# Kernel tuning notes

Hardware: AMD Instinct MI355X
Metric: run time of the kernel (lower is better)

## Reference

```python
import jax, jax.numpy as jnp
import numpy as np
from jax import lax

INPUT_SIZE = 512
THRESHOLD = 0.5
IOU_TH = 0.3
MAX_ROIS = 32   # py_cpu_nms(...)[:32]
ROI = 7
NEG = jnp.float32(-1e30)


def _make_anchors(fh, fw, stride):
    # 3 scales x 3 ratios = 9 anchors per cell, laid out in (h, w, anchor)
    # order to match permute(0,2,3,1).view(-1) of the conv heads.
    scales = np.array([32.0, 64.0, 128.0])
    ratios = np.array([0.5, 1.0, 2.0])
    ws = (scales[:, None] * np.sqrt(ratios)[None, :]).reshape(-1)
    hs = (scales[:, None] / np.sqrt(ratios)[None, :]).reshape(-1)
    cy = (np.arange(fh) + 0.5) * stride
    cx = (np.arange(fw) + 0.5) * stride
    CX, CY = np.meshgrid(cx, cy)
    CX = CX[..., None]; CY = CY[..., None]
    a = np.stack([CX - ws / 2, CY - hs / 2, CX + ws / 2, CY + hs / 2], axis=-1)
    return jnp.asarray(a.reshape(-1, 4), jnp.float32)


def setup_inputs() -> dict:
    key = jax.random.key(0)
    k1, k2, k3 = jax.random.split(key, 3)
    B, C, FH, FW, A, stride = 4, 256, 64, 64, 9, 8
    featureMap = jax.random.normal(k1, (B, C, FH, FW), jnp.float32)
    # small init so sigmoid scores spread across threshold and exp(tw) stays sane
    w_cls = jax.random.normal(k2, (A, C, 3, 3), jnp.float32) * 0.05
    w_loc = jax.random.normal(k3, (4 * A, C, 3, 3), jnp.float32) * 0.01
    prior_anchor = _make_anchors(FH, FW, stride)
    return {"featureMap": featureMap, "prior_anchor": prior_anchor,
            "w_cls": w_cls, "w_loc": w_loc, "stride": stride}


def _conv(x, w):
    return lax.conv_general_dilated(x, w, (1, 1), "SAME",
                                    dimension_numbers=("NCHW", "OIHW", "NCHW"))


def _decode(loc, anchors):
    aw = anchors[:, 2] - anchors[:, 0]
    ah = anchors[:, 3] - anchors[:, 1]
    acx = anchors[:, 0] + 0.5 * aw
    acy = anchors[:, 1] + 0.5 * ah
    cx = acx + loc[:, 0] * aw
    cy = acy + loc[:, 1] * ah
    w = aw * jnp.exp(loc[:, 2])
    h = ah * jnp.exp(loc[:, 3])
    return jnp.stack([cx - 0.5 * w, cy - 0.5 * h, cx + 0.5 * w, cy + 0.5 * h], axis=1)


def _iou_one(box, boxes):
    xx1 = jnp.maximum(box[0], boxes[:, 0]); yy1 = jnp.maximum(box[1], boxes[:, 1])
    xx2 = jnp.minimum(box[2], boxes[:, 2]); yy2 = jnp.minimum(box[3], boxes[:, 3])
    inter = jnp.clip(xx2 - xx1, 0) * jnp.clip(yy2 - yy1, 0)
    a1 = (box[2] - box[0]) * (box[3] - box[1])
    a2 = (boxes[:, 2] - boxes[:, 0]) * (boxes[:, 3] - boxes[:, 1])
    return inter / (a1 + a2 - inter + 1e-9)


def _nms(boxes, scores, valid):
    # greedy NMS, fixed MAX_ROIS rounds (== sort-by-score py_cpu_nms + [:32])
    N = scores.shape[0]
    s0 = jnp.where(valid, scores, -1.0)

    def body(i, carry):
        s, picks, ok = carry
        idx = jnp.argmax(s)
        good = s[idx] > 0.0
        picks = picks.at[i].set(idx.astype(jnp.int32))
        ok = ok.at[i].set(good)
        sup = (_iou_one(boxes[idx], boxes) > IOU_TH) | (jnp.arange(N) == idx)
        return (jnp.where(sup, -1.0, s), picks, ok)

    _, picks, ok = lax.fori_loop(
        0, MAX_ROIS, body,
        (s0, jnp.zeros(MAX_ROIS, jnp.int32), jnp.zeros(MAX_ROIS, bool)))
    return picks, ok


def _ceil_div(a, b):
    return -(-a // b)


def _adaptive_maxpool(feat, box):
    # feat: [C, FH, FW]; box: int32 [x1, y1, x2, y2] in feature-map coords.
    # Faithful F.adaptive_max_pool2d bins: start=floor(i*h/7), end=ceil((i+1)*h/7).
    FH, FW = feat.shape[1], feat.shape[2]
    x1, y1, x2, y2 = box[0], box[1], box[2], box[3]
    h = y2 - y1; w = x2 - x1
    i = jnp.arange(ROI)
    rs = y1 + (i * h) // ROI; re = y1 + _ceil_div((i + 1) * h, ROI)
    cs = x1 + (i * w) // ROI; ce = x1 + _ceil_div((i + 1) * w, ROI)
    hh = jnp.arange(FH); ww = jnp.arange(FW)
    rm = jnp.where((hh >= rs[:, None]) & (hh < re[:, None]), 0.0, NEG)  # [7, FH]
    cm = jnp.where((ww >= cs[:, None]) & (ww < ce[:, None]), 0.0, NEG)  # [7, FW]
    t = jnp.max(feat[None] + rm[:, None, :, None], axis=2)              # [7, C, FW]
    out = jnp.max(t[:, None] + cm[None, :, None, :], axis=3)            # [7, 7, C]
    return jnp.transpose(out, (2, 0, 1))                                # [C, 7, 7]


def reference(featureMap, prior_anchor, w_cls, w_loc, stride):
    B, C, FH, FW = featureMap.shape
    cls = jax.nn.sigmoid(_conv(featureMap, w_cls))                      # [B, A, FH, FW]
    cls = jnp.transpose(cls, (0, 2, 3, 1)).reshape(B, -1)               # [B, N]
    loc = jnp.transpose(_conv(featureMap, w_loc), (0, 2, 3, 1)).reshape(B, -1, 4)
    boxes = jax.vmap(_decode, in_axes=(0, None))(loc, prior_anchor)     # [B, N, 4]
    boxes = jnp.clip(boxes, 0.0, float(INPUT_SIZE))                     # clamp(0, input_size)
    valid = (cls > THRESHOLD) \
          & (boxes[..., 2] - boxes[..., 0] >= 2 * stride) \
          & (boxes[..., 3] - boxes[..., 1] >= 2 * stride)
    picks, ok = jax.vmap(_nms)(boxes, cls, valid)                       # [B, 32]
    sel_boxes = jnp.take_along_axis(boxes, picks[..., None], axis=1)    # [B, 32, 4]
    sel_scores = jnp.take_along_axis(cls, picks, axis=1)                # [B, 32]
    eval_boxes = jnp.where(
        ok[..., None],
        jnp.concatenate([sel_boxes, sel_scores[..., None]], axis=-1), 0.0)
    # src_coordinate.int() / stride -> integer feature-map coords
    ib = sel_boxes.astype(jnp.int32) // stride
    fx1 = jnp.clip(ib[..., 0], 0, FW - 1); fy1 = jnp.clip(ib[..., 1], 0, FH - 1)
    fx2 = jnp.clip(ib[..., 2], fx1 + 1, FW); fy2 = jnp.clip(ib[..., 3], fy1 + 1, FH)
    fb = jnp.stack([fx1, fy1, fx2, fy2], axis=-1).reshape(-1, 4)        # [B*32, 4]
    img = jnp.repeat(jnp.arange(B), MAX_ROIS)
    rois = lax.map(lambda a: _adaptive_maxpool(featureMap[a[1]], a[0]), (fb, img))
    rois = jnp.where(ok.reshape(-1)[:, None, None, None], rois, 0.0)    # [B*32, 256, 7, 7]
    return eval_boxes, ok, rois
```

## Files before the change

### kernel.cpp

```cpp
#include <hip/hip_runtime.h>
#include <hip/hip_bf16.h>

#define FHH 64
#define FWW 64
#define CIN 256
#define NB 4
#define NA 9
#define NANCH 36864
#define NPOS 4096
#define OC_TOTAL 45
#define OCP 48
#define MAXROIS 32
#define ROI 7
#define NEGV -1e30f
#define NCHUNK 576
#define NTH 16
#define CAP 1024

typedef unsigned long long u64;

__device__ __constant__ const float TH_LADDER[NTH] = {
    0.9999f, 0.9998f, 0.9995f, 0.999f, 0.998f, 0.997f, 0.995f, 0.993f,
    0.99f, 0.987f, 0.984f, 0.98f, 0.975f, 0.97f, 0.96f, 0.0f};

__device__ __forceinline__ void pick_threshold(
    const int* __restrict__ gcnt, int b, int cap,
    float* T, int* C, int* V, int* frc)
{
    int bestc = 0; float bt = TH_LADDER[0];
#pragma unroll
    for (int i = 0; i < NTH; ++i) {
        int c = gcnt[b * NTH + i];
        if (c <= cap && c > bestc) { bestc = c; bt = TH_LADDER[i]; }
    }
    int f = (gcnt[b * NTH + 0] > cap) ? 1 : 0;
    if (f) { bestc = cap; bt = TH_LADDER[0]; }
    *T = bt; *C = bestc; *V = gcnt[b * NTH + NTH - 1]; *frc = f;
}

__global__ __launch_bounds__(256) void wtrans_kernel(
    const float* __restrict__ wcls,
    const float* __restrict__ wloc,
    float* __restrict__ wT,
    int* __restrict__ gcnt)
{
    if (blockIdx.x == 0 && threadIdx.x < NB * NTH) gcnt[threadIdx.x] = 0;
    int idx = blockIdx.x * 256 + threadIdx.x;
    int o = idx % 48;
    int rest = idx / 48;
    int tap = rest % 9;
    int c = rest / 9;
    float v = 0.f;
    if (o < OC_TOTAL) {
        v = (o < NA) ? wcls[((size_t)o * CIN + c) * 9 + tap]
                     : wloc[((size_t)(o - NA) * CIN + c) * 9 + tap];
    }
    wT[idx] = v;
}

__global__ __launch_bounds__(256) void conv_kernel(
    const float* __restrict__ feat,
    const float* __restrict__ wT,
    float* __restrict__ partial,
    int nkg, int cpk)
{
    __shared__ float flds[16][18][20];

    int blk = blockIdx.x;
    int low = blk & 7;
    int rest = blk >> 3;
    int kg = rest % nkg;
    int uhi = rest / nkg;
    int unit = uhi * 8 + low;
    int b = unit >> 4;
    int tile = unit & 15;

    int ty0 = (tile >> 2) * 16;
    int tx0 = (tile & 3) * 16;

    int pb = threadIdx.x & 63;
    int q = __builtin_amdgcn_readfirstlane(threadIdx.x >> 6);
    int ry0 = (pb >> 3) * 2;
    int rx0 = (pb & 7) * 2;

    int cbase = kg * cpk;

    float acc[2][2][12];
#pragma unroll
    for (int py = 0; py < 2; ++py)
#pragma unroll
        for (int px = 0; px < 2; ++px)
#pragma unroll
            for (int o = 0; o < 12; ++o) acc[py][px][o] = 0.f;

    for (int c0 = 0; c0 < cpk; c0 += 16) {
        __syncthreads();
        for (int idx = threadIdx.x; idx < 16 * 324; idx += 256) {
            int c = idx / 324;
            int r = idx - c * 324;
            int y = r / 18;
            int x = r - y * 18;
            int gy = ty0 + y - 1;
            int gx = tx0 + x - 1;
            float v = 0.f;
            if ((unsigned)gy < FHH && (unsigned)gx < FWW)
                v = feat[((size_t)(b * CIN + cbase + c0 + c) * FHH + gy) * FWW + gx];
            flds[c][y][x] = v;
        }
        __syncthreads();

        const float* wq = wT + (size_t)(cbase + c0) * 432 + q * 12;
        for (int c = 0; c < 16; ++c) {
            float f[4][4];
#pragma unroll
            for (int r = 0; r < 4; ++r) {
                float2 a0 = *(const float2*)&flds[c][ry0 + r][rx0];
                float2 a1 = *(const float2*)&flds[c][ry0 + r][rx0 + 2];
                f[r][0] = a0.x; f[r][1] = a0.y; f[r][2] = a1.x; f[r][3] = a1.y;
            }
#pragma unroll
            for (int tap = 0; tap < 9; ++tap) {
                int dy = tap / 3, dx = tap % 3;
                const float* wp = wq + (c * 9 + tap) * 48;
                float w[12];
#pragma unroll
                for (int o = 0; o < 12; ++o) w[o] = wp[o];
#pragma unroll
                for (int py = 0; py < 2; ++py)
#pragma unroll
                for (int px = 0; px < 2; ++px) {
                    float fv = f[py + dy][px + dx];
#pragma unroll
                    for (int o = 0; o < 12; ++o)
                        acc[py][px][o] += fv * w[o];
                }
            }
        }
    }

    float* pout = partial + ((size_t)kg * NB + b) * OCP * NPOS;
#pragma unroll
    for (int o = 0; o < 12; ++o) {
        int oo = q * 12 + o;
        if (oo >= OC_TOTAL) continue;
        float* op = pout + (size_t)oo * NPOS;
#pragma unroll
        for (int py = 0; py < 2; ++py)
#pragma unroll
        for (int px = 0; px < 2; ++px) {
            int pos = (ty0 + ry0 + py) * FWW + (tx0 + rx0 + px);
            op[pos] = acc[py][px][o];
        }
    }
}

__global__ __launch_bounds__(256) void decode_kernel(
    const float* __restrict__ partial,
    const float* __restrict__ anchors,
    const int* __restrict__ stridep,
    float* __restrict__ boxes,
    float* __restrict__ scores,
    int* __restrict__ gcnt,
    int* __restrict__ gcount,
    int nkg)
{
    __shared__ int hcnt[NTH];
    if (threadIdx.x < NTH) hcnt[threadIdx.x] = 0;
    if (blockIdx.x == 0 && threadIdx.x < NB) gcount[threadIdx.x] = 0;
    __syncthreads();

    int t = blockIdx.x * 256 + threadIdx.x;
    int pos = t & (NPOS - 1);
    int ba = t >> 12;
    int b = ba / 9;
    int a = ba - b * 9;

    float cls = 0.f, l0 = 0.f, l1 = 0.f, l2 = 0.f, l3 = 0.f;
    for (int kg = 0; kg < nkg; ++kg) {
        const float* pk = partial + ((size_t)kg * NB + b) * OCP * NPOS;
        cls += pk[(size_t)a * NPOS + pos];
        l0 += pk[(size_t)(NA + a * 4 + 0) * NPOS + pos];
        l1 += pk[(size_t)(NA + a * 4 + 1) * NPOS + pos];
        l2 += pk[(size_t)(NA + a * 4 + 2) * NPOS + pos];
        l3 += pk[(size_t)(NA + a * 4 + 3) * NPOS + pos];
    }

    float sig = 1.f / (1.f + expf(-cls));
    int n = pos * NA + a;
    const float* an = anchors + (size_t)n * 4;
    float ax1 = an[0], ay1 = an[1], ax2 = an[2], ay2 = an[3];
    float aw = ax2 - ax1, ah = ay2 - ay1;
    float acx = ax1 + 0.5f * aw, acy = ay1 + 0.5f * ah;
    float cx = acx + l0 * aw;
    float cy = acy + l1 * ah;
    float w = aw * expf(l2);
    float h = ah * expf(l3);
    float x1 = fminf(fmaxf(cx - 0.5f * w, 0.f), 512.f);
    float y1 = fminf(fmaxf(cy - 0.5f * h, 0.f), 512.f);
    float x2 = fminf(fmaxf(cx + 0.5f * w, 0.f), 512.f);
    float y2 = fminf(fmaxf(cy + 0.5f * h, 0.f), 512.f);
    int stride = stridep[0];
    float msz = 2.f * (float)stride;
    bool valid = (sig > 0.5f) && ((x2 - x1) >= msz) && ((y2 - y1) >= msz);
    ((float4*)boxes)[(size_t)b * NANCH + n] = make_float4(x1, y1, x2, y2);
    scores[(size_t)b * NANCH + n] = valid ? sig : -1.0f;

#pragma unroll
    for (int i = 0; i < NTH; ++i) {
        u64 mb = __ballot(valid && sig >= TH_LADDER[i]);
        if ((threadIdx.x & 63) == 0 && mb)
            atomicAdd(&hcnt[i], (int)__popcll(mb));
    }
    __syncthreads();
    if (threadIdx.x < NTH && hcnt[threadIdx.x])
        atomicAdd(&gcnt[b * NTH + threadIdx.x], hcnt[threadIdx.x]);
}

__global__ __launch_bounds__(256) void nms_compact_kernel(
    const float* __restrict__ scores,
    const int* __restrict__ gcnt,
    int* __restrict__ gcount,
    u64* __restrict__ candkey,
    int cap)
{
    __shared__ int lcnt;
    __shared__ int wbase[4];
    __shared__ int gbase;
    int t = blockIdx.x * 256 + threadIdx.x;
    int b = t / NANCH;
    int j = t - b * NANCH;
    int lane = threadIdx.x & 63;
    int w = threadIdx.x >> 6;
    if (threadIdx.x == 0) lcnt = 0;
    __syncthreads();

    float T; int C, V, frc;
    pick_threshold(gcnt, b, cap, &T, &C, &V, &frc);

    float v = scores[t];
    bool p = (v > 0.f) && (v >= T);
    u64 m = __ballot(p);
    int cnt = (int)__popcll(m);
    if (lane == 0) wbase[w] = atomicAdd(&lcnt, cnt);
    __syncthreads();
    if (threadIdx.x == 0) gbase = lcnt ? atomicAdd(&gcount[b], lcnt) : 0;
    __syncthreads();
    if (p) {
        int off = (int)__popcll(m & ((1ULL << lane) - 1ULL));
        int slot = gbase + wbase[w] + off;
        if (slot < cap)
            candkey[(size_t)b * cap + slot] =
                ((u64)__float_as_uint(v) << 32) | (unsigned int)(~j);
    }
}

__device__ __forceinline__ void write_outputs(
    int b, int i, bool okv, int idx, float sc,
    const float4* Bb4, const int* stridep,
    float* d_out, int* ifb, int* iok)
{
    float4 bb = Bb4[idx];
    float* eb = d_out + ((size_t)b * MAXROIS + i) * 5;
    eb[0] = okv ? bb.x : 0.f;
    eb[1] = okv ? bb.y : 0.f;
    eb[2] = okv ? bb.z : 0.f;
    eb[3] = okv ? bb.w : 0.f;
    eb[4] = okv ? sc : 0.f;
    d_out[NB * MAXROIS * 5 + b * MAXROIS + i] = okv ? 1.f : 0.f;
    int st = stridep[0];
    int fx1 = min(max(((int)bb.x) / st, 0), FWW - 1);
    int fy1 = min(max(((int)bb.y) / st, 0), FHH - 1);
    int fx2 = min(max(((int)bb.z) / st, fx1 + 1), FWW);
    int fy2 = min(max(((int)bb.w) / st, fy1 + 1), FHH);
    int r = b * MAXROIS + i;
    ifb[r * 4 + 0] = fx1;
    ifb[r * 4 + 1] = fy1;
    ifb[r * 4 + 2] = fx2;
    ifb[r * 4 + 3] = fy2;
    iok[r] = okv ? 1 : 0;
}

__global__ __launch_bounds__(512) void nms_sortscan_kernel(
    const u64* __restrict__ candkey,
    const float* __restrict__ boxes,
    const int* __restrict__ gcnt,
    const int* __restrict__ stridep,
    float* __restrict__ d_out,
    int* __restrict__ ifb, int* __restrict__ iok, int* __restrict__ flag,
    int cap)
{
    __shared__ u64 skey[CAP];
    __shared__ float4 box_l[CAP];
    __shared__ u64 mask[CAP / 64];
    __shared__ int picks[MAXROIS];
    __shared__ int np_sh;

    int b = blockIdx.x;
    int tid = threadIdx.x;
    int lane = tid & 63;
    if (tid == 0) np_sh = 0;

    float T; int C, V, frc;
    pick_threshold(gcnt, b, cap, &T, &C, &V, &frc);

    int CSZ = 64;
    while (CSZ < C) CSZ <<= 1;

    for (int j = tid; j < CSZ; j += 512)
        skey[j] = (j < C) ? candkey[(size_t)b * cap + j] : 0ULL;

    int prev_cross = 1;
    for (int kk = 2; kk <= CSZ; kk <<= 1) {
        for (int jj = kk >> 1; jj > 0; jj >>= 1) {
            int cross = (jj >= 128) ? 1 : 0;
            if (cross || prev_cross) __syncthreads();
            for (int tt = tid; tt < (CSZ >> 1); tt += 512) {
                int i = ((tt & ~(jj - 1)) << 1) | (tt & (jj - 1));
                int l = i + jj;
                u64 a = skey[i], c2 = skey[l];
                bool up = ((i & kk) == 0);
                bool sw = up ? (a < c2) : (a > c2);
                if (sw) { skey[i] = c2; skey[l] = a; }
            }
            prev_cross = cross;
        }
    }
    __syncthreads();

    const float4* Bb4 = (const float4*)(boxes + (size_t)b * NANCH * 4);
    for (int j = tid; j < C; j += 512) {
        int id = (int)(~((unsigned int)(skey[j] & 0xFFFFFFFFULL)));
        box_l[j] = Bb4[id];
    }
    if (tid < CAP / 64) {
        int base = tid * 64;
        u64 m0;
        if (base >= C) m0 = ~0ULL;
        else if (base + 64 > C) m0 = ~((1ULL << (C - base)) - 1ULL);
        else m0 = 0ULL;
        mask[tid] = m0;
    }
    __syncthreads();

    for (int round = 0; round < MAXROIS; ++round) {
        u64 mw = (lane < CAP / 64) ? mask[lane] : ~0ULL;
        int bpos = __ffsll((u64)(~mw));
        int cand = bpos ? lane * 64 + bpos - 1 : 0x7FFFFFFF;
#pragma unroll
        for (int off = 32; off >= 1; off >>= 1)
            cand = min(cand, __shfl_xor(cand, off));
        int pj = cand;
        if (pj == 0x7FFFFFFF) break;
        if (tid == 0) {
            picks[round] = pj;
            np_sh = round + 1;
            atomicOr(&mask[pj >> 6], 1ULL << (pj & 63));
        }
        float4 pb = box_l[pj];
        float parea = (pb.z - pb.x) * (pb.w - pb.y);
        int j0 = tid * 2;
        u64 curm = mask[tid >> 5];
        u64 addm = 0ULL;
#pragma unroll
        for (int d = 0; d < 2; ++d) {
            int j = j0 + d;
            if (j > pj && j < C && !((curm >> (j & 63)) & 1ULL)) {
                float4 bb2 = box_l[j];
                float xx1 = fmaxf(pb.x, bb2.x), yy1 = fmaxf(pb.y, bb2.y);
                float xx2 = fminf(pb.z, bb2.z), yy2 = fminf(pb.w, bb2.w);
                float inter = fmaxf(xx2 - xx1, 0.f) * fmaxf(yy2 - yy1, 0.f);
                float a2 = (bb2.z - bb2.x) * (bb2.w - bb2.y);
                float iou = inter / (parea + a2 - inter + 1e-9f);
                if (iou > 0.3f) addm |= 1ULL << (j & 63);
            }
        }
        if (addm) atomicOr(&mask[tid >> 5], addm);
        __syncthreads();
    }
    __syncthreads();

    int np = np_sh;
    bool need_fb = frc || (np < MAXROIS && V > C);
    if (tid == 0) flag[b] = need_fb ? 1 : 0;
    if (!need_fb && tid < MAXROIS) {
        int i = tid;
        bool okv = i < np;
        int slot = okv ? picks[i] : 0;
        u64 k = skey[slot];
        int idx = okv ? (int)(~((unsigned int)(k & 0xFFFFFFFFULL))) : 0;
        float sc = okv ? __uint_as_float((unsigned int)(k >> 32)) : 0.f;
        write_outputs(b, i, okv, idx, sc, Bb4, stridep, d_out, ifb, iok);
    }
}

__global__ __launch_bounds__(1024) void nms_fallback_kernel(
    const float* __restrict__ boxes,
    const float* __restrict__ scores,
    const int* __restrict__ stridep,
    float* __restrict__ d_out,
    int* __restrict__ ifb,
    int* __restrict__ iok,
    const int* __restrict__ flag)
{
    __shared__ float s[NANCH];
    __shared__ float2 cmax[NCHUNK];
    __shared__ int   picks_sh[MAXROIS];
    __shared__ float pscore_sh[MAXROIS];

    int b = blockIdx.x;
    if (flag[b] == 0) return;

    const float4* Bb4 = (const float4*)(boxes + (size_t)b * NANCH * 4);
    const float* Sb = scores + (size_t)b * NANCH;
    int lane = threadIdx.x & 63;
    int w = threadIdx.x >> 6;

    for (int k = 0; k < 36; ++k) {
        int ch = w * 36 + k;
        int j = ch * 64 + lane;
        float v = Sb[j];
        s[j] = v;
        float bv = v; int bi = j;
#pragma unroll
        for (int off = 32; off >= 1; off >>= 1) {
            float ov = __shfl_xor(bv, off);
            int   oi = __shfl_xor(bi, off);
            if (ov > bv || (ov == bv && oi < bi)) { bv = ov; bi = oi; }
        }
        if (lane == 0) cmax[ch] = make_float2(bv, __int_as_float(bi));
    }
    __syncthreads();
    if (w != 0) return;

    float px1 = 0.f, py1 = 0.f, px2 = 0.f, py2 = 0.f, parea = 0.f;
    int np = 0;
    while (np < MAXROIS) {
        float bv = -2.f; int bi = 0x7fffffff;
#pragma unroll
        for (int k = 0; k < 9; ++k) {
            float2 cm = cmax[lane * 9 + k];
            int ci = __float_as_int(cm.y);
            if (cm.x > bv || (cm.x == bv && ci < bi)) { bv = cm.x; bi = ci; }
        }
#pragma unroll
        for (int off = 32; off >= 1; off >>= 1) {
            float ov = __shfl_xor(bv, off);
            int   oi = __shfl_xor(bi, off);
            if (ov > bv || (ov == bv && oi < bi)) { bv = ov; bi = oi; }
        }
        if (bv <= 0.f) break;
        int fi = bi; float fs = bv;

        float4 cbb = Bb4[fi];

        bool sup = false;
        if (lane < np) {
            float xx1 = fmaxf(px1, cbb.x), yy1 = fmaxf(py1, cbb.y);
            float xx2 = fminf(px2, cbb.z), yy2 = fminf(py2, cbb.w);
            float inter = fmaxf(xx2 - xx1, 0.f) * fmaxf(yy2 - yy1, 0.f);
            float a2 = (cbb.z - cbb.x) * (cbb.w - cbb.y);
            float iou = inter / (parea + a2 - inter + 1e-9f);
            sup = iou > 0.3f;
        }
        u64 m = __ballot(sup);

        int ch = fi >> 6;
        int j = ch * 64 + lane;
        float sv = (j == fi) ? -1.f : s[j];
        if (j == fi) s[j] = -1.f;
        float nv = sv; int ni = j;
#pragma unroll
        for (int off = 32; off >= 1; off >>= 1) {
            float ov = __shfl_xor(nv, off);
            int   oi = __shfl_xor(ni, off);
            if (ov > nv || (ov == nv && oi < ni)) { nv = ov; ni = oi; }
        }
        if (lane == 0) cmax[ch] = make_float2(nv, __int_as_float(ni));

        if (m == 0ULL) {
            if (lane == np) {
                px1 = cbb.x; py1 = cbb.y; px2 = cbb.z; py2 = cbb.w;
                parea = (px2 - px1) * (py2 - py1);
            }
            picks_sh[np] = fi;
            pscore_sh[np] = fs;
            ++np;
        }
    }

    if (lane < MAXROIS) {
        int i = lane;
        bool okv = i < np;
        int idx = okv ? picks_sh[i] : 0;
        float sc = okv ? pscore_sh[i] : 0.f;
        write_outputs(b, i, okv, idx, sc, Bb4, stridep, d_out, ifb, iok);
    }
}

__global__ __launch_bounds__(256) void roi_kernel(
    const float* __restrict__ feat,
    const int* __restrict__ ifb,
    const int* __restrict__ iok,
    float* __restrict__ out_rois)
{
    int t = blockIdx.x * 256 + threadIdx.x;
    int bin = t % 49;
    int rc = t / 49;
    int c = rc & 255;
    int r = rc >> 8;
    int i = bin / 7;
    int j = bin - i * 7;

    if (!iok[r]) { out_rois[t] = 0.f; return; }

    int x1 = ifb[r * 4 + 0];
    int y1 = ifb[r * 4 + 1];
    int x2 = ifb[r * 4 + 2];
    int y2 = ifb[r * 4 + 3];
    int h = y2 - y1;
    int w = x2 - x1;
    int b = r >> 5;

    int rs = y1 + (i * h) / ROI;
    int re = y1 + ((i + 1) * h + ROI - 1) / ROI;
    int cs = x1 + (j * w) / ROI;
    int ce = x1 + ((j + 1) * w + ROI - 1) / ROI;

    const float* F = feat + (size_t)(b * CIN + c) * NPOS;
    float m = NEGV;
    for (int y = rs; y < re; ++y) {
        const float* row = F + y * FWW;
        for (int x = cs; x < ce; ++x) m = fmaxf(m, row[x]);
    }
    out_rois[t] = m;
}

extern "C" void kernel_launch(void* const* d_in, const int* in_sizes, int n_in,
                              void* d_out, int out_size, void* d_ws, size_t ws_size,
                              hipStream_t stream) {
    const float* feat    = (const float*)d_in[0];
    const float* anchors = (const float*)d_in[1];
    const float* wcls    = (const float*)d_in[2];
    const float* wloc    = (const float*)d_in[3];
    const int*   stridep = (const int*)d_in[4];
    float* out = (float*)d_out;
    float* ws  = (float*)d_ws;

    const size_t P1 = (size_t)NB * OCP * NPOS;
    const size_t WTN = 256 * 9 * 48;
    const int cap = CAP;

    auto need = [&](int nk) -> size_t {
        size_t f = P1 * nk
                 + 589824 + 147456 + WTN
                 + (size_t)NB * cap * 2
                 + 2048;
        return f * 4;
    };
    int nkg = 16;
    if (ws_size < need(16)) {
        if (ws_size >= need(8)) { nkg = 8; }
        else { nkg = 4; }
    }

    float* partial   = ws;
    float* boxes     = partial + P1 * nkg;
    float* scores    = boxes + (size_t)NB * NANCH * 4;
    float* wT        = scores + (size_t)NB * NANCH;
    u64*   candkey   = (u64*)(wT + WTN);
    float* tailf     = (float*)(candkey + (size_t)NB * cap);
    int*   ifb       = (int*)tailf;
    int*   iok       = ifb + 512;
    int*   flag      = iok + 128;
    int*   gcnt      = flag + 4;
    int*   gcount    = gcnt + 64;

    wtrans_kernel<<<432, 256, 0, stream>>>(wcls, wloc, wT, gcnt);
    conv_kernel<<<64 * nkg, 256, 0, stream>>>(feat, wT, partial, nkg, CIN / nkg);
    decode_kernel<<<(NB * NANCH) / 256, 256, 0, stream>>>(partial, anchors, stridep, boxes, scores, gcnt, gcount, nkg);
    nms_compact_kernel<<<(NB * NANCH) / 256, 256, 0, stream>>>(scores, gcnt, gcount, candkey, cap);
    nms_sortscan_kernel<<<NB, 512, 0, stream>>>(candkey, boxes, gcnt, stridep, out, ifb, iok, flag, cap);
    nms_fallback_kernel<<<NB, 1024, 0, stream>>>(boxes, scores, stridep, out, ifb, iok, flag);
    roi_kernel<<<(NB * MAXROIS * CIN * 49) / 256, 256, 0, stream>>>(feat, ifb, iok, out + NB * MAXROIS * 5 + NB * MAXROIS);
}
```

Before: 137.2 us.

## Stage each feature-map channel plane in shared memory for ROI max pooling

The ROI pooling kernel now assigns one block per (image, channel) pair. The block loads the full 64x64 plane into LDS with float4 reads, then computes all 32 ROIs x 49 bins from LDS instead of each thread doing scattered global reads. This trades redundant, uncoalesced global traffic for one coalesced 16KB load per plane. Output writes become strided by channel, and the whole plane is loaded even when few ROIs are valid.

```diff
diff --git a/kernel.cpp b/kernel.cpp
--- a/kernel.cpp
+++ b/kernel.cpp
@@ -503,36 +503,48 @@
     const int* __restrict__ iok,
     float* __restrict__ out_rois)
 {
-    int t = blockIdx.x * 256 + threadIdx.x;
-    int bin = t % 49;
-    int rc = t / 49;
-    int c = rc & 255;
-    int r = rc >> 8;
-    int i = bin / 7;
-    int j = bin - i * 7;
-
-    if (!iok[r]) { out_rois[t] = 0.f; return; }
-
-    int x1 = ifb[r * 4 + 0];
-    int y1 = ifb[r * 4 + 1];
-    int x2 = ifb[r * 4 + 2];
-    int y2 = ifb[r * 4 + 3];
-    int h = y2 - y1;
-    int w = x2 - x1;
-    int b = r >> 5;
-
-    int rs = y1 + (i * h) / ROI;
-    int re = y1 + ((i + 1) * h + ROI - 1) / ROI;
-    int cs = x1 + (j * w) / ROI;
-    int ce = x1 + ((j + 1) * w + ROI - 1) / ROI;
-
-    const float* F = feat + (size_t)(b * CIN + c) * NPOS;
-    float m = NEGV;
-    for (int y = rs; y < re; ++y) {
-        const float* row = F + y * FWW;
-        for (int x = cs; x < ce; ++x) m = fmaxf(m, row[x]);
-    }
-    out_rois[t] = m;
+    __shared__ float plane[NPOS];
+    __shared__ int sifb[MAXROIS * 4];
+    __shared__ int siok[MAXROIS];
+
+    int bc = blockIdx.x;
+    int b = bc >> 8;
+    int c = bc & 255;
+
+    const float4* F4 = (const float4*)(feat + (size_t)bc * NPOS);
+    float4* P4 = (float4*)plane;
+    for (int i = threadIdx.x; i < NPOS / 4; i += 256)
+        P4[i] = F4[i];
+    if (threadIdx.x < MAXROIS * 4) sifb[threadIdx.x] = ifb[b * MAXROIS * 4 + threadIdx.x];
+    if (threadIdx.x < MAXROIS) siok[threadIdx.x] = iok[b * MAXROIS + threadIdx.x];
+    __syncthreads();
+
+    for (int t = threadIdx.x; t < MAXROIS * 49; t += 256) {
+        int r = t / 49;
+        int bin = t - r * 49;
+        int i = bin / 7;
+        int j = bin - i * 7;
+        float outv = 0.f;
+        if (siok[r]) {
+            int x1 = sifb[r * 4 + 0];
+            int y1 = sifb[r * 4 + 1];
+            int x2 = sifb[r * 4 + 2];
+            int y2 = sifb[r * 4 + 3];
+            int h = y2 - y1;
+            int w = x2 - x1;
+            int rs = y1 + (i * h) / ROI;
+            int re = y1 + ((i + 1) * h + ROI - 1) / ROI;
+            int cs = x1 + (j * w) / ROI;
+            int ce = x1 + ((j + 1) * w + ROI - 1) / ROI;
+            float m = NEGV;
+            for (int y = rs; y < re; ++y) {
+                const float* row = plane + y * FWW;
+                for (int x = cs; x < ce; ++x) m = fmaxf(m, row[x]);
+            }
+            outv = m;
+        }
+        out_rois[((size_t)(b * MAXROIS + r) * CIN + c) * 49 + bin] = outv;
+    }
 }
 
 extern "C" void kernel_launch(void* const* d_in, const int* in_sizes, int n_in,
@@ -581,5 +593,5 @@
     nms_compact_kernel<<<(NB * NANCH) / 256, 256, 0, stream>>>(scores, gcnt, gcount, candkey, cap);
     nms_sortscan_kernel<<<NB, 512, 0, stream>>>(candkey, boxes, gcnt, stridep, out, ifb, iok, flag, cap);
     nms_fallback_kernel<<<NB, 1024, 0, stream>>>(boxes, scores, stridep, out, ifb, iok, flag);
-    roi_kernel<<<(NB * MAXROIS * CIN * 49) / 256, 256, 0, stream>>>(feat, ifb, iok, out + NB * MAXROIS * 5 + NB * MAXROIS);
-}
+    roi_kernel<<<NB * CIN, 256, 0, stream>>>(feat, ifb, iok, out + NB * MAXROIS * 5 + NB * MAXROIS);
+}
```

Measured after the change: 137.6 us. About the same (+0.3%).
